# Performance work log

Measured on AMD Instinct MI355X. Metric: run time of the kernel, lower is better.

## Reference

```python
import jax, jax.numpy as jnp
import numpy as np

BATCH, AMINOS, ATOMS = 16, 1024, 8192
AMINO_DIM = EMBED_DIM = ATOM_DIM = 128


def setup_inputs() -> dict:
    key = jax.random.key(0)
    ks = jax.random.split(key, 7)
    x = jax.random.normal(ks[0], (BATCH, AMINOS, AMINO_DIM, 3), dtype=jnp.float32)
    embeddings = jax.random.normal(ks[1], (1, ATOMS, EMBED_DIM), dtype=jnp.float32)
    # sorted gather index emulates per-residue expand/concat in aminos_copy
    amino_idx = jnp.sort(jax.random.randint(ks[2], (ATOMS,), 0, AMINOS))
    s_in = 1.0 / np.sqrt(AMINO_DIM)
    s_e = 1.0 / np.sqrt(EMBED_DIM)
    W_emb = jax.random.normal(ks[3], (EMBED_DIM, EMBED_DIM), dtype=jnp.float32) * s_e
    b_emb = jax.random.normal(ks[4], (EMBED_DIM,), dtype=jnp.float32) * s_e
    W_in = jax.random.normal(ks[5], (EMBED_DIM, AMINO_DIM), dtype=jnp.float32) * s_in
    W_out = jax.random.normal(ks[6], (ATOM_DIM, EMBED_DIM), dtype=jnp.float32) * s_e
    return {"x": x, "embeddings": embeddings, "amino_idx": amino_idx,
            "W_emb": W_emb, "b_emb": b_emb, "W_in": W_in, "W_out": W_out}


def reference(x, embeddings, amino_idx, W_emb, b_emb, W_in, W_out):
    # modulation = lin_embed(embeddings): (1, atoms, E)
    mod = jnp.einsum('oae,fe->oaf', embeddings, W_emb) + b_emb
    # lin_in over channel dim, independent of vector index: (b, aminos, E, 3)
    h = jnp.einsum('bacv,ec->baev', x, W_in)
    # aminos_copy as a single gather along the amino axis -> (b, atoms, E, 3)
    g = jnp.take(h, amino_idx, axis=1)
    # modulate (broadcast modulation over batch and vector index)
    y = mod[..., None] * g
    # lin_out over channel dim: (b, atoms, atom_dim, 3)
    return jnp.einsum('baev,de->badv', y, W_out)
```

## Files before the change

### kernel.cpp

```cpp
#include <hip/hip_runtime.h>
#include <hip/hip_bf16.h>

#define AMINOS 1024
#define ATOMS  8192
#define DIM    128

typedef __attribute__((ext_vector_type(8))) short  short8;
typedef __attribute__((ext_vector_type(4))) float  f32x4;

__device__ __forceinline__ unsigned short f2bf(float f) {
    unsigned int u; __builtin_memcpy(&u, &f, 4);
    unsigned int r = (u + 0x7fffu + ((u >> 16) & 1u)) >> 16;
    return (unsigned short)r;
}
__device__ __forceinline__ float bf2f(unsigned short us) {
    unsigned int x = ((unsigned int)us) << 16;
    float f; __builtin_memcpy(&f, &x, 4);
    return f;
}

__device__ __forceinline__ int swz(int row, int ch) { return row * 16 + (ch ^ (row & 7)); }

__global__ __launch_bounds__(256) void k_convert(const float* __restrict__ wemb,
                                                 const float* __restrict__ win,
                                                 const float* __restrict__ wout,
                                                 unsigned short* __restrict__ dst) {
    int i = blockIdx.x * 256 + threadIdx.x;
    const float* src = (i < 16384) ? wemb : ((i < 32768) ? win : wout);
    dst[i] = f2bf(src[i & 16383]);
}

__global__ __launch_bounds__(256) void k_mod(const float* __restrict__ emb,
                                             const unsigned short* __restrict__ wembB,
                                             const float* __restrict__ bemb,
                                             float* __restrict__ mod) {
    __shared__ short Al[64 * 128];
    __shared__ short Bl[128 * 128];
    const int tid = threadIdx.x;
    const int a0 = blockIdx.x * 64;

    #pragma unroll
    for (int t = 0; t < 4; ++t) {
        int task = tid + t * 256;
        int row = task >> 4, ch = task & 15;
        const f32x4* p = (const f32x4*)(emb + (a0 + row) * 128 + ch * 8);
        f32x4 lo = p[0], hi = p[1];
        short8 v;
        v[0]=f2bf(lo[0]); v[1]=f2bf(lo[1]); v[2]=f2bf(lo[2]); v[3]=f2bf(lo[3]);
        v[4]=f2bf(hi[0]); v[5]=f2bf(hi[1]); v[6]=f2bf(hi[2]); v[7]=f2bf(hi[3]);
        *(short8*)&Al[swz(row, ch) * 8] = v;
    }
    #pragma unroll
    for (int t = 0; t < 8; ++t) {
        int cc = tid + t * 256;
        int rr = cc >> 4, ch = cc & 15;
        short8 v = *(const short8*)(wembB + cc * 8);
        *(short8*)&Bl[swz(rr, ch) * 8] = v;
    }
    __syncthreads();

    const int lane = tid & 63, w = tid >> 6;
    const int col = lane & 15, kg = lane >> 4;
    const int rt = w;

    short8 af[4];
    #pragma unroll
    for (int ks = 0; ks < 4; ++ks) {
        int r = rt * 16 + col;
        af[ks] = *(const short8*)&Al[swz(r, ks * 4 + kg) * 8];
    }
    f32x4 acc[8];
    #pragma unroll
    for (int ct = 0; ct < 8; ++ct) { acc[ct][0]=0.f; acc[ct][1]=0.f; acc[ct][2]=0.f; acc[ct][3]=0.f; }

    #pragma unroll
    for (int ct = 0; ct < 8; ++ct) {
        int r = ct * 16 + col;
        #pragma unroll
        for (int ks = 0; ks < 4; ++ks) {
            short8 bf = *(const short8*)&Bl[swz(r, ks * 4 + kg) * 8];
            acc[ct] = __builtin_amdgcn_mfma_f32_16x16x32_bf16(af[ks], bf, acc[ct], 0, 0, 0);
        }
    }
    #pragma unroll
    for (int ct = 0; ct < 8; ++ct) {
        int f = ct * 16 + col;
        float bb = bemb[f];
        #pragma unroll
        for (int reg = 0; reg < 4; ++reg) {
            int r = rt * 16 + kg * 4 + reg;
            mod[(a0 + r) * 128 + f] = acc[ct][reg] + bb;
        }
    }
}

__global__ __launch_bounds__(256) void k_h(const float* __restrict__ x,
                                           const unsigned short* __restrict__ winB,
                                           unsigned short* __restrict__ h) {
    __shared__ short Al[48 * 128];
    __shared__ short Bl[128 * 128];
    const int tid = threadIdx.x;
    const int g0 = blockIdx.x * 16;

    {
        int p = tid >> 4, ch = tid & 15;
        const f32x4* q = (const f32x4*)(x + (g0 + p) * 384 + ch * 24);
        f32x4 q0 = q[0], q1 = q[1], q2 = q[2], q3 = q[3], q4 = q[4], q5 = q[5];
        float e[24];
        *(f32x4*)&e[0]  = q0; *(f32x4*)&e[4]  = q1; *(f32x4*)&e[8]  = q2;
        *(f32x4*)&e[12] = q3; *(f32x4*)&e[16] = q4; *(f32x4*)&e[20] = q5;
        #pragma unroll
        for (int v = 0; v < 3; ++v) {
            short8 vv;
            #pragma unroll
            for (int i = 0; i < 8; ++i) vv[i] = (short)f2bf(e[v + 3 * i]);
            *(short8*)&Al[swz(p * 3 + v, ch) * 8] = vv;
        }
    }
    #pragma unroll
    for (int t = 0; t < 8; ++t) {
        int cc = tid + t * 256;
        int rr = cc >> 4, ch = cc & 15;
        short8 v = *(const short8*)(winB + cc * 8);
        *(short8*)&Bl[swz(rr, ch) * 8] = v;
    }
    __syncthreads();

    const int lane = tid & 63, w = tid >> 6;
    const int col = lane & 15, kg = lane >> 4;

    short8 af[3][4];
    #pragma unroll
    for (int rt = 0; rt < 3; ++rt) {
        int r = rt * 16 + col;
        #pragma unroll
        for (int ks = 0; ks < 4; ++ks) af[rt][ks] = *(const short8*)&Al[swz(r, ks * 4 + kg) * 8];
    }
    f32x4 acc[3][2];
    #pragma unroll
    for (int rt = 0; rt < 3; ++rt)
        #pragma unroll
        for (int c2 = 0; c2 < 2; ++c2) { acc[rt][c2][0]=0.f; acc[rt][c2][1]=0.f; acc[rt][c2][2]=0.f; acc[rt][c2][3]=0.f; }

    #pragma unroll
    for (int c2 = 0; c2 < 2; ++c2) {
        int ct = w * 2 + c2;
        int r = ct * 16 + col;
        #pragma unroll
        for (int ks = 0; ks < 4; ++ks) {
            short8 bf = *(const short8*)&Bl[swz(r, ks * 4 + kg) * 8];
            #pragma unroll
            for (int rt = 0; rt < 3; ++rt)
                acc[rt][c2] = __builtin_amdgcn_mfma_f32_16x16x32_bf16(af[rt][ks], bf, acc[rt][c2], 0, 0, 0);
        }
    }
    #pragma unroll
    for (int rt = 0; rt < 3; ++rt) {
        #pragma unroll
        for (int c2 = 0; c2 < 2; ++c2) {
            int e = (w * 2 + c2) * 16 + col;
            #pragma unroll
            for (int reg = 0; reg < 4; ++reg) {
                int R = rt * 16 + kg * 4 + reg;
                int p = R / 3, v = R - 3 * p;
                h[((g0 + p) * 3 + v) * 128 + e] = f2bf(acc[rt][c2][reg]);
            }
        }
    }
}

__global__ __launch_bounds__(256) void k_out(const unsigned short* __restrict__ h,
                                             const float* __restrict__ mod,
                                             const int* __restrict__ idx,
                                             const unsigned short* __restrict__ woutB,
                                             float* __restrict__ out) {
    __shared__ short Al[48 * 128];
    __shared__ short Bl[128 * 128];
    const int tid = threadIdx.x;
    const int b = blockIdx.x & 15;
    const int a0 = (blockIdx.x >> 4) * 16;

    #pragma unroll
    for (int t = 0; t < 3; ++t) {
        int task = tid + t * 256;
        int row = task >> 4, ch = task & 15;
        int al = row / 3, v = row - 3 * al;
        int a = a0 + al;
        int ia = idx[a];
        short8 hv = *(const short8*)(h + ((b * AMINOS + ia) * 3 + v) * 128 + ch * 8);
        const f32x4* mp = (const f32x4*)(mod + a * 128 + ch * 8);
        f32x4 m0 = mp[0], m1 = mp[1];
        short8 vv;
        vv[0]=(short)f2bf(bf2f((unsigned short)hv[0]) * m0[0]);
        vv[1]=(short)f2bf(bf2f((unsigned short)hv[1]) * m0[1]);
        vv[2]=(short)f2bf(bf2f((unsigned short)hv[2]) * m0[2]);
        vv[3]=(short)f2bf(bf2f((unsigned short)hv[3]) * m0[3]);
        vv[4]=(short)f2bf(bf2f((unsigned short)hv[4]) * m1[0]);
        vv[5]=(short)f2bf(bf2f((unsigned short)hv[5]) * m1[1]);
        vv[6]=(short)f2bf(bf2f((unsigned short)hv[6]) * m1[2]);
        vv[7]=(short)f2bf(bf2f((unsigned short)hv[7]) * m1[3]);
        *(short8*)&Al[swz(row, ch) * 8] = vv;
    }
    #pragma unroll
    for (int t = 0; t < 8; ++t) {
        int cc = tid + t * 256;
        int rr = cc >> 4, ch = cc & 15;
        short8 v = *(const short8*)(woutB + cc * 8);
        *(short8*)&Bl[swz(rr, ch) * 8] = v;
    }
    __syncthreads();

    const int lane = tid & 63, w = tid >> 6;
    const int col = lane & 15, kg = lane >> 4;

    short8 af[3][4];
    #pragma unroll
    for (int rt = 0; rt < 3; ++rt) {
        int r = rt * 16 + col;
        #pragma unroll
        for (int ks = 0; ks < 4; ++ks) af[rt][ks] = *(const short8*)&Al[swz(r, ks * 4 + kg) * 8];
    }
    f32x4 acc[3][2];
    #pragma unroll
    for (int rt = 0; rt < 3; ++rt)
        #pragma unroll
        for (int c2 = 0; c2 < 2; ++c2) { acc[rt][c2][0]=0.f; acc[rt][c2][1]=0.f; acc[rt][c2][2]=0.f; acc[rt][c2][3]=0.f; }

    #pragma unroll
    for (int c2 = 0; c2 < 2; ++c2) {
        int ct = w * 2 + c2;
        int r = ct * 16 + col;
        #pragma unroll
        for (int ks = 0; ks < 4; ++ks) {
            short8 bf = *(const short8*)&Bl[swz(r, ks * 4 + kg) * 8];
            #pragma unroll
            for (int rt = 0; rt < 3; ++rt)
                acc[rt][c2] = __builtin_amdgcn_mfma_f32_16x16x32_bf16(af[rt][ks], bf, acc[rt][c2], 0, 0, 0);
        }
    }
    #pragma unroll
    for (int rt = 0; rt < 3; ++rt) {
        #pragma unroll
        for (int c2 = 0; c2 < 2; ++c2) {
            int d = (w * 2 + c2) * 16 + col;
            #pragma unroll
            for (int reg = 0; reg < 4; ++reg) {
                int R = rt * 16 + kg * 4 + reg;
                int al = R / 3, v = R - 3 * al;
                int a = a0 + al;
                out[((b * ATOMS + a) * 128 + d) * 3 + v] = acc[rt][c2][reg];
            }
        }
    }
}

extern "C" void kernel_launch(void* const* d_in, const int* in_sizes, int n_in,
                              void* d_out, int out_size, void* d_ws, size_t ws_size,
                              hipStream_t stream) {
    const float* x    = (const float*)d_in[0];
    const float* emb  = (const float*)d_in[1];
    const int*   idx  = (const int*)d_in[2];
    const float* wemb = (const float*)d_in[3];
    const float* bemb = (const float*)d_in[4];
    const float* win  = (const float*)d_in[5];
    const float* wout = (const float*)d_in[6];
    float* out = (float*)d_out;

    char* ws = (char*)d_ws;
    float*          mod = (float*)ws;
    unsigned short* h   = (unsigned short*)(ws + (4u << 20));
    unsigned short* wB  = (unsigned short*)(ws + 16777216u);

    k_convert<<<192, 256, 0, stream>>>(wemb, win, wout, wB);
    k_mod    <<<128, 256, 0, stream>>>(emb, wB, bemb, mod);
    k_h      <<<1024, 256, 0, stream>>>(x, wB + 16384, h);
    k_out    <<<8192, 256, 0, stream>>>(h, mod, idx, wB + 32768, out);
}
```

Measured before the change: 263.2 us.

## Loop four tiles per block reusing weight fragments and stage coalesced output stores via LDS

```diff
diff --git a/kernel.cpp b/kernel.cpp
--- a/kernel.cpp
+++ b/kernel.cpp
@@ -3,7 +3,6 @@
 
 #define AMINOS 1024
 #define ATOMS  8192
-#define DIM    128
 
 typedef __attribute__((ext_vector_type(8))) short  short8;
 typedef __attribute__((ext_vector_type(4))) float  f32x4;
@@ -65,10 +64,8 @@
 
     short8 af[4];
     #pragma unroll
-    for (int ks = 0; ks < 4; ++ks) {
-        int r = rt * 16 + col;
-        af[ks] = *(const short8*)&Al[swz(r, ks * 4 + kg) * 8];
-    }
+    for (int ks = 0; ks < 4; ++ks) af[ks] = *(const short8*)&Al[swz(rt * 16 + col, ks * 4 + kg) * 8];
+
     f32x4 acc[8];
     #pragma unroll
     for (int ct = 0; ct < 8; ++ct) { acc[ct][0]=0.f; acc[ct][1]=0.f; acc[ct][2]=0.f; acc[ct][3]=0.f; }
@@ -99,24 +96,9 @@
                                            unsigned short* __restrict__ h) {
     __shared__ short Al[48 * 128];
     __shared__ short Bl[128 * 128];
+    unsigned short* Hs = (unsigned short*)Bl;
     const int tid = threadIdx.x;
-    const int g0 = blockIdx.x * 16;
-
-    {
-        int p = tid >> 4, ch = tid & 15;
-        const f32x4* q = (const f32x4*)(x + (g0 + p) * 384 + ch * 24);
-        f32x4 q0 = q[0], q1 = q[1], q2 = q[2], q3 = q[3], q4 = q[4], q5 = q[5];
-        float e[24];
-        *(f32x4*)&e[0]  = q0; *(f32x4*)&e[4]  = q1; *(f32x4*)&e[8]  = q2;
-        *(f32x4*)&e[12] = q3; *(f32x4*)&e[16] = q4; *(f32x4*)&e[20] = q5;
-        #pragma unroll
-        for (int v = 0; v < 3; ++v) {
-            short8 vv;
-            #pragma unroll
-            for (int i = 0; i < 8; ++i) vv[i] = (short)f2bf(e[v + 3 * i]);
-            *(short8*)&Al[swz(p * 3 + v, ch) * 8] = vv;
-        }
-    }
+
     #pragma unroll
     for (int t = 0; t < 8; ++t) {
         int cc = tid + t * 256;
@@ -129,43 +111,73 @@
     const int lane = tid & 63, w = tid >> 6;
     const int col = lane & 15, kg = lane >> 4;
 
-    short8 af[3][4];
-    #pragma unroll
-    for (int rt = 0; rt < 3; ++rt) {
-        int r = rt * 16 + col;
-        #pragma unroll
-        for (int ks = 0; ks < 4; ++ks) af[rt][ks] = *(const short8*)&Al[swz(r, ks * 4 + kg) * 8];
-    }
-    f32x4 acc[3][2];
-    #pragma unroll
-    for (int rt = 0; rt < 3; ++rt)
-        #pragma unroll
-        for (int c2 = 0; c2 < 2; ++c2) { acc[rt][c2][0]=0.f; acc[rt][c2][1]=0.f; acc[rt][c2][2]=0.f; acc[rt][c2][3]=0.f; }
-
+    short8 bfr[2][4];
     #pragma unroll
     for (int c2 = 0; c2 < 2; ++c2) {
-        int ct = w * 2 + c2;
-        int r = ct * 16 + col;
-        #pragma unroll
-        for (int ks = 0; ks < 4; ++ks) {
-            short8 bf = *(const short8*)&Bl[swz(r, ks * 4 + kg) * 8];
-            #pragma unroll
-            for (int rt = 0; rt < 3; ++rt)
-                acc[rt][c2] = __builtin_amdgcn_mfma_f32_16x16x32_bf16(af[rt][ks], bf, acc[rt][c2], 0, 0, 0);
-        }
-    }
-    #pragma unroll
-    for (int rt = 0; rt < 3; ++rt) {
-        #pragma unroll
-        for (int c2 = 0; c2 < 2; ++c2) {
-            int e = (w * 2 + c2) * 16 + col;
-            #pragma unroll
-            for (int reg = 0; reg < 4; ++reg) {
-                int R = rt * 16 + kg * 4 + reg;
-                int p = R / 3, v = R - 3 * p;
-                h[((g0 + p) * 3 + v) * 128 + e] = f2bf(acc[rt][c2][reg]);
+        int r = (w * 2 + c2) * 16 + col;
+        #pragma unroll
+        for (int ks = 0; ks < 4; ++ks) bfr[c2][ks] = *(const short8*)&Bl[swz(r, ks * 4 + kg) * 8];
+    }
+
+    for (int it = 0; it < 4; ++it) {
+        const int g0 = blockIdx.x * 64 + it * 16;
+        {
+            int p = tid >> 4, ch = tid & 15;
+            const f32x4* q = (const f32x4*)(x + (size_t)(g0 + p) * 384 + ch * 24);
+            f32x4 q0 = q[0], q1 = q[1], q2 = q[2], q3 = q[3], q4 = q[4], q5 = q[5];
+            float e[24];
+            *(f32x4*)&e[0]  = q0; *(f32x4*)&e[4]  = q1; *(f32x4*)&e[8]  = q2;
+            *(f32x4*)&e[12] = q3; *(f32x4*)&e[16] = q4; *(f32x4*)&e[20] = q5;
+            #pragma unroll
+            for (int v = 0; v < 3; ++v) {
+                short8 vv;
+                #pragma unroll
+                for (int i = 0; i < 8; ++i) vv[i] = (short)f2bf(e[v + 3 * i]);
+                *(short8*)&Al[swz(p * 3 + v, ch) * 8] = vv;
             }
         }
+        __syncthreads();
+
+        f32x4 acc[3][2];
+        #pragma unroll
+        for (int rt = 0; rt < 3; ++rt)
+            #pragma unroll
+            for (int c2 = 0; c2 < 2; ++c2) { acc[rt][c2][0]=0.f; acc[rt][c2][1]=0.f; acc[rt][c2][2]=0.f; acc[rt][c2][3]=0.f; }
+
+        #pragma unroll
+        for (int rt = 0; rt < 3; ++rt) {
+            int r = rt * 16 + col;
+            short8 af[4];
+            #pragma unroll
+            for (int ks = 0; ks < 4; ++ks) af[ks] = *(const short8*)&Al[swz(r, ks * 4 + kg) * 8];
+            #pragma unroll
+            for (int ks = 0; ks < 4; ++ks)
+                #pragma unroll
+                for (int c2 = 0; c2 < 2; ++c2)
+                    acc[rt][c2] = __builtin_amdgcn_mfma_f32_16x16x32_bf16(af[ks], bfr[c2][ks], acc[rt][c2], 0, 0, 0);
+        }
+        __syncthreads();
+
+        #pragma unroll
+        for (int rt = 0; rt < 3; ++rt)
+            #pragma unroll
+            for (int c2 = 0; c2 < 2; ++c2) {
+                int e = (w * 2 + c2) * 16 + col;
+                #pragma unroll
+                for (int reg = 0; reg < 4; ++reg) {
+                    int R = rt * 16 + kg * 4 + reg;
+                    Hs[R * 128 + e] = f2bf(acc[rt][c2][reg]);
+                }
+            }
+        __syncthreads();
+
+        unsigned short* hb = h + (size_t)g0 * 3 * 128;
+        #pragma unroll
+        for (int t2 = 0; t2 < 3; ++t2) {
+            int c = tid + t2 * 256;
+            *(short8*)(hb + c * 8) = *(const short8*)&Hs[c * 8];
+        }
+        __syncthreads();
     }
 }
 
@@ -176,31 +188,11 @@
                                              float* __restrict__ out) {
     __shared__ short Al[48 * 128];
     __shared__ short Bl[128 * 128];
+    float* Os = (float*)Bl;
     const int tid = threadIdx.x;
     const int b = blockIdx.x & 15;
-    const int a0 = (blockIdx.x >> 4) * 16;
-
-    #pragma unroll
-    for (int t = 0; t < 3; ++t) {
-        int task = tid + t * 256;
-        int row = task >> 4, ch = task & 15;
-        int al = row / 3, v = row - 3 * al;
-        int a = a0 + al;
-        int ia = idx[a];
-        short8 hv = *(const short8*)(h + ((b * AMINOS + ia) * 3 + v) * 128 + ch * 8);
-        const f32x4* mp = (const f32x4*)(mod + a * 128 + ch * 8);
-        f32x4 m0 = mp[0], m1 = mp[1];
-        short8 vv;
-        vv[0]=(short)f2bf(bf2f((unsigned short)hv[0]) * m0[0]);
-        vv[1]=(short)f2bf(bf2f((unsigned short)hv[1]) * m0[1]);
-        vv[2]=(short)f2bf(bf2f((unsigned short)hv[2]) * m0[2]);
-        vv[3]=(short)f2bf(bf2f((unsigned short)hv[3]) * m0[3]);
-        vv[4]=(short)f2bf(bf2f((unsigned short)hv[4]) * m1[0]);
-        vv[5]=(short)f2bf(bf2f((unsigned short)hv[5]) * m1[1]);
-        vv[6]=(short)f2bf(bf2f((unsigned short)hv[6]) * m1[2]);
-        vv[7]=(short)f2bf(bf2f((unsigned short)hv[7]) * m1[3]);
-        *(short8*)&Al[swz(row, ch) * 8] = vv;
-    }
+    const int abase = (blockIdx.x >> 4) * 64;
+
     #pragma unroll
     for (int t = 0; t < 8; ++t) {
         int cc = tid + t * 256;
@@ -213,44 +205,80 @@
     const int lane = tid & 63, w = tid >> 6;
     const int col = lane & 15, kg = lane >> 4;
 
-    short8 af[3][4];
-    #pragma unroll
-    for (int rt = 0; rt < 3; ++rt) {
-        int r = rt * 16 + col;
-        #pragma unroll
-        for (int ks = 0; ks < 4; ++ks) af[rt][ks] = *(const short8*)&Al[swz(r, ks * 4 + kg) * 8];
-    }
-    f32x4 acc[3][2];
-    #pragma unroll
-    for (int rt = 0; rt < 3; ++rt)
-        #pragma unroll
-        for (int c2 = 0; c2 < 2; ++c2) { acc[rt][c2][0]=0.f; acc[rt][c2][1]=0.f; acc[rt][c2][2]=0.f; acc[rt][c2][3]=0.f; }
-
+    short8 bfr[2][4];
     #pragma unroll
     for (int c2 = 0; c2 < 2; ++c2) {
-        int ct = w * 2 + c2;
-        int r = ct * 16 + col;
-        #pragma unroll
-        for (int ks = 0; ks < 4; ++ks) {
-            short8 bf = *(const short8*)&Bl[swz(r, ks * 4 + kg) * 8];
-            #pragma unroll
-            for (int rt = 0; rt < 3; ++rt)
-                acc[rt][c2] = __builtin_amdgcn_mfma_f32_16x16x32_bf16(af[rt][ks], bf, acc[rt][c2], 0, 0, 0);
-        }
-    }
-    #pragma unroll
-    for (int rt = 0; rt < 3; ++rt) {
-        #pragma unroll
-        for (int c2 = 0; c2 < 2; ++c2) {
-            int d = (w * 2 + c2) * 16 + col;
-            #pragma unroll
-            for (int reg = 0; reg < 4; ++reg) {
-                int R = rt * 16 + kg * 4 + reg;
-                int al = R / 3, v = R - 3 * al;
-                int a = a0 + al;
-                out[((b * ATOMS + a) * 128 + d) * 3 + v] = acc[rt][c2][reg];
+        int r = (w * 2 + c2) * 16 + col;
+        #pragma unroll
+        for (int ks = 0; ks < 4; ++ks) bfr[c2][ks] = *(const short8*)&Bl[swz(r, ks * 4 + kg) * 8];
+    }
+
+    for (int it = 0; it < 4; ++it) {
+        const int a0 = abase + it * 16;
+        #pragma unroll
+        for (int t = 0; t < 3; ++t) {
+            int task = tid + t * 256;
+            int row = task >> 4, ch = task & 15;
+            int al = row / 3, v = row - 3 * al;
+            int a = a0 + al;
+            int ia = idx[a];
+            short8 hv = *(const short8*)(h + (size_t)((b * AMINOS + ia) * 3 + v) * 128 + ch * 8);
+            const f32x4* mp = (const f32x4*)(mod + a * 128 + ch * 8);
+            f32x4 m0 = mp[0], m1 = mp[1];
+            short8 vv;
+            vv[0]=(short)f2bf(bf2f((unsigned short)hv[0]) * m0[0]);
+            vv[1]=(short)f2bf(bf2f((unsigned short)hv[1]) * m0[1]);
+            vv[2]=(short)f2bf(bf2f((unsigned short)hv[2]) * m0[2]);
+            vv[3]=(short)f2bf(bf2f((unsigned short)hv[3]) * m0[3]);
+            vv[4]=(short)f2bf(bf2f((unsigned short)hv[4]) * m1[0]);
+            vv[5]=(short)f2bf(bf2f((unsigned short)hv[5]) * m1[1]);
+            vv[6]=(short)f2bf(bf2f((unsigned short)hv[6]) * m1[2]);
+            vv[7]=(short)f2bf(bf2f((unsigned short)hv[7]) * m1[3]);
+            *(short8*)&Al[swz(row, ch) * 8] = vv;
+        }
+        __syncthreads();
+
+        f32x4 acc[3][2];
+        #pragma unroll
+        for (int rt = 0; rt < 3; ++rt)
+            #pragma unroll
+            for (int c2 = 0; c2 < 2; ++c2) { acc[rt][c2][0]=0.f; acc[rt][c2][1]=0.f; acc[rt][c2][2]=0.f; acc[rt][c2][3]=0.f; }
+
+        #pragma unroll
+        for (int rt = 0; rt < 3; ++rt) {
+            int r = rt * 16 + col;
+            short8 af[4];
+            #pragma unroll
+            for (int ks = 0; ks < 4; ++ks) af[ks] = *(const short8*)&Al[swz(r, ks * 4 + kg) * 8];
+            #pragma unroll
+            for (int ks = 0; ks < 4; ++ks)
+                #pragma unroll
+                for (int c2 = 0; c2 < 2; ++c2)
+                    acc[rt][c2] = __builtin_amdgcn_mfma_f32_16x16x32_bf16(af[ks], bfr[c2][ks], acc[rt][c2], 0, 0, 0);
+        }
+        __syncthreads();
+
+        #pragma unroll
+        for (int rt = 0; rt < 3; ++rt)
+            #pragma unroll
+            for (int c2 = 0; c2 < 2; ++c2) {
+                int d = (w * 2 + c2) * 16 + col;
+                #pragma unroll
+                for (int reg = 0; reg < 4; ++reg) {
+                    int R = rt * 16 + kg * 4 + reg;
+                    int al = R / 3, v = R - 3 * al;
+                    Os[al * 384 + d * 3 + v] = acc[rt][c2][reg];
+                }
             }
-        }
+        __syncthreads();
+
+        float* ob = out + ((size_t)b * ATOMS + a0) * 384;
+        #pragma unroll
+        for (int t2 = 0; t2 < 6; ++t2) {
+            int c = tid + t2 * 256;
+            *(f32x4*)(ob + c * 4) = *(const f32x4*)&Os[c * 4];
+        }
+        __syncthreads();
     }
 }
 
@@ -273,6 +301,6 @@
 
     k_convert<<<192, 256, 0, stream>>>(wemb, win, wout, wB);
     k_mod    <<<128, 256, 0, stream>>>(emb, wB, bemb, mod);
-    k_h      <<<1024, 256, 0, stream>>>(x, wB + 16384, h);
-    k_out    <<<8192, 256, 0, stream>>>(h, mod, idx, wB + 32768, out);
-}
+    k_h      <<<256, 256, 0, stream>>>(x, wB + 16384, h);
+    k_out    <<<2048, 256, 0, stream>>>(h, mod, idx, wB + 32768, out);
+}
```

Result: faster. 245.4 us (-6.7%).
